# Kernel optimization log

Hardware: AMD Instinct MI355X
Metric: run time of the kernel (lower is better)

The kernel has to match this reference:

```python
import jax, jax.numpy as jnp
import numpy as np

B, T, D, H, E = 32, 512, 768, 12, 6  # batch, seq(=input_size), n_embd, num_heads, per-head dim
DFF = 4 * D
EPS = 1e-5


def setup_inputs() -> dict:
    key = jax.random.key(0)
    ks = jax.random.split(key, 10)
    s = 0.02
    return {
        "x": jax.random.normal(ks[0], (B, T, D), jnp.float32),
        "Wq": jax.random.normal(ks[1], (H, D, E), jnp.float32) * s,
        "Wk": jax.random.normal(ks[2], (H, D, E), jnp.float32) * s,
        "Wv": jax.random.normal(ks[3], (H, D, E), jnp.float32) * s,
        "Wo": jax.random.normal(ks[4], (H * E, D), jnp.float32) * s,
        "bo": jnp.zeros((D,), jnp.float32),
        "W1": jax.random.normal(ks[5], (D, DFF), jnp.float32) * s,
        "b1": jnp.zeros((DFF,), jnp.float32),
        "W2": jax.random.normal(ks[6], (DFF, D), jnp.float32) * s,
        "b2": jnp.zeros((D,), jnp.float32),
        "g1": jnp.ones((D,), jnp.float32),
        "beta1": jnp.zeros((D,), jnp.float32),
        "g2": jnp.ones((D,), jnp.float32),
        "beta2": jnp.zeros((D,), jnp.float32),
    }


def _layernorm(x, g, b):
    m = jnp.mean(x, axis=-1, keepdims=True)
    v = jnp.var(x, axis=-1, keepdims=True)  # biased, matches torch LayerNorm
    return (x - m) * jax.lax.rsqrt(v + EPS) * g + b


def reference(x, Wq, Wk, Wv, Wo, bo, W1, b1, W2, b2, g1, beta1, g2, beta2):
    # --- pre-LN multi-head causal attention (dropout = identity, eval mode) ---
    xn = _layernorm(x, g1, beta1)
    q = jnp.einsum("btd,hde->bhte", xn, Wq)
    k = jnp.einsum("btd,hde->bhte", xn, Wk)
    v = jnp.einsum("btd,hde->bhte", xn, Wv)
    scores = jnp.einsum("bhte,bhse->bhts", q, k) * (E ** -0.5)
    causal = jnp.tril(jnp.ones((T, T), dtype=bool))
    scores = jnp.where(causal, scores, -jnp.inf)
    w = jax.nn.softmax(scores, axis=-1)
    o = jnp.einsum("bhts,bhse->bhte", w, v)
    o = o.transpose(0, 2, 1, 3).reshape(B, T, H * E)  # concat heads -> [B,T,72]
    x = x + o @ Wo + bo
    # --- pre-LN feed-forward ---
    y = _layernorm(x, g2, beta2)
    ff = jax.nn.relu(y @ W1 + b1) @ W2 + b2
    return x + ff
```

## Files before the change

kernel.cpp:

```cpp
#include <hip/hip_runtime.h>
#include <hip/hip_bf16.h>

#define BT 16384
#define DIM 768
#define NH 12
#define DFF 3072

typedef __attribute__((ext_vector_type(8))) short short8;
typedef __attribute__((ext_vector_type(4))) float floatx4;
typedef __attribute__((ext_vector_type(4))) unsigned short ushort4b;

using bf16 = __hip_bfloat16;

static __device__ __forceinline__ float b2f(bf16 v) { return __bfloat162float(v); }
static __device__ __forceinline__ bf16 f2b(float v) { return __float2bfloat16(v); }
static __device__ __forceinline__ float blo(unsigned int u) { return __uint_as_float(u << 16); }
static __device__ __forceinline__ float bhi(unsigned int u) { return __uint_as_float(u & 0xffff0000u); }

static __device__ __forceinline__ void gload_lds16(const void* g, void* l) {
    __builtin_amdgcn_global_load_lds(
        (const __attribute__((address_space(1))) unsigned int*)g,
        (__attribute__((address_space(3))) unsigned int*)l, 16, 0, 0);
}

__global__ __launch_bounds__(256) void prep_kernel(
    const float* __restrict__ Wq, const float* __restrict__ Wk, const float* __restrict__ Wv,
    const float* __restrict__ Wo, const float* __restrict__ W1, const float* __restrict__ W2,
    bf16* __restrict__ wqkv, bf16* __restrict__ wo_t,
    bf16* __restrict__ w1t, bf16* __restrict__ w2t)
{
    const int z = blockIdx.z;
    if (z == 2) {
        int i = (blockIdx.y * 96 + blockIdx.x) * 256 + threadIdx.x;
        const int S0 = 256 * 768, S1 = 768 * 96;
        if (i < S0) {
            int c = i / 768, dd = i % 768;
            float v = 0.f;
            if (c < 216) {
                int sel = c / 72, cc = c % 72, h = cc / 6, e = cc % 6;
                const float* W = (sel == 0) ? Wq : (sel == 1) ? Wk : Wv;
                v = W[((size_t)h * 768 + dd) * 6 + e];
            }
            wqkv[i] = f2b(v);
        } else if ((i -= S0) < S1) {
            int n = i / 96, r = i % 96;
            wo_t[i] = f2b(r < 72 ? Wo[r * 768 + n] : 0.f);
        }
        return;
    }
    const float* in = z ? W2 : W1;
    bf16* out = z ? w2t : w1t;
    const int R = z ? 3072 : 768, C = z ? 768 : 3072;
    const int bx = z ? blockIdx.y : blockIdx.x;
    const int by = z ? blockIdx.x : blockIdx.y;
    __shared__ float t[32][33];
    int c0 = bx * 32, r0 = by * 32;
    int cx = threadIdx.x & 31, ry = threadIdx.x >> 5;
#pragma unroll
    for (int j = 0; j < 4; j++)
        t[ry + j * 8][cx] = in[(size_t)(r0 + ry + j * 8) * C + c0 + cx];
    __syncthreads();
    int rx = cx, cy = ry;
#pragma unroll
    for (int j = 0; j < 4; j++)
        out[(size_t)(c0 + cy + j * 8) * R + r0 + rx] = f2b(t[rx][cy + j * 8]);
}

__global__ __launch_bounds__(192) void ln_kernel(
    const float* __restrict__ x, const float* __restrict__ g, const float* __restrict__ be,
    bf16* __restrict__ out)
{
    int row = blockIdx.x;
    int tid = threadIdx.x;
    const float4* xr = (const float4*)(x + (size_t)row * DIM);
    float4 v = xr[tid];
    float s = v.x + v.y + v.z + v.w;
    float s2 = v.x * v.x + v.y * v.y + v.z * v.z + v.w * v.w;
#pragma unroll
    for (int off = 32; off; off >>= 1) {
        s += __shfl_down(s, off);
        s2 += __shfl_down(s2, off);
    }
    __shared__ float red[6];
    int wv = tid >> 6, ln = tid & 63;
    if (ln == 0) { red[wv] = s; red[3 + wv] = s2; }
    __syncthreads();
    float ts = red[0] + red[1] + red[2];
    float ts2 = red[3] + red[4] + red[5];
    float mean = ts * (1.f / 768.f);
    float var = ts2 * (1.f / 768.f) - mean * mean;
    float rstd = rsqrtf(var + 1e-5f);
    int c = tid * 4;
    float o0 = (v.x - mean) * rstd * g[c + 0] + be[c + 0];
    float o1 = (v.y - mean) * rstd * g[c + 1] + be[c + 1];
    float o2 = (v.z - mean) * rstd * g[c + 2] + be[c + 2];
    float o3 = (v.w - mean) * rstd * g[c + 3] + be[c + 3];
    bf16 h0 = f2b(o0), h1 = f2b(o1), h2 = f2b(o2), h3 = f2b(o3);
    ushort4b pk;
    pk[0] = *(unsigned short*)&h0; pk[1] = *(unsigned short*)&h1;
    pk[2] = *(unsigned short*)&h2; pk[3] = *(unsigned short*)&h3;
    *(ushort4b*)(out + (size_t)row * DIM + c) = pk;
}

template <int NSLAB, bool RELU, bool BIAS, bool RES, bool BF16OUT>
__global__ __launch_bounds__(256) void gemm_kernel(
    const bf16* __restrict__ A, const bf16* __restrict__ Bt,
    const float* __restrict__ bias, const float* __restrict__ res,
    void* __restrict__ Cv, int M, int N, int K)
{
    constexpr int SMEM_BYTES = BF16OUT ? (128 * 136 * 2) : (NSLAB * 2 * 128 * 32 * 2);
    __shared__ __align__(16) char smem[SMEM_BYTES];
    bf16* lA = (bf16*)smem;
    bf16* lB = lA + NSLAB * 128 * 32;

    const int tid = threadIdx.x;
    const int bm = blockIdx.x * 128;
    const int bn = blockIdx.y * 128;
    const int wave = tid >> 6, lane = tid & 63;
    const int wm = (wave >> 1) * 64, wn = (wave & 1) * 64;
    const int quad = lane >> 4, l16 = lane & 15;
    const int lrow = lane >> 2;
    const int lkc = (lane & 3) * 8;

    floatx4 acc[4][4] = {};

    for (int k0 = 0; k0 < K; k0 += NSLAB * 32) {
#pragma unroll
        for (int s = 0; s < NSLAB; s++) {
#pragma unroll
            for (int it = 0; it < 2; it++) {
                int r = wave * 32 + it * 16;
                gload_lds16(A + (size_t)(bm + r + lrow) * K + k0 + s * 32 + lkc,
                            lA + s * 4096 + r * 32);
                gload_lds16(Bt + (size_t)(bn + r + lrow) * K + k0 + s * 32 + lkc,
                            lB + s * 4096 + r * 32);
            }
        }
        __syncthreads();
#pragma unroll
        for (int s = 0; s < NSLAB; s++) {
            short8 af[4], bfr[4];
#pragma unroll
            for (int mt = 0; mt < 4; mt++)
                af[mt] = *(const short8*)(lA + s * 4096 + (wm + mt * 16 + l16) * 32 + quad * 8);
#pragma unroll
            for (int nt = 0; nt < 4; nt++)
                bfr[nt] = *(const short8*)(lB + s * 4096 + (wn + nt * 16 + l16) * 32 + quad * 8);
#pragma unroll
            for (int mt = 0; mt < 4; mt++)
#pragma unroll
                for (int nt = 0; nt < 4; nt++)
                    acc[mt][nt] = __builtin_amdgcn_mfma_f32_16x16x32_bf16(af[mt], bfr[nt], acc[mt][nt], 0, 0, 0);
        }
        __syncthreads();
    }

    if constexpr (BF16OUT) {
        bf16* ltile = (bf16*)smem;
#pragma unroll
        for (int mt = 0; mt < 4; mt++) {
#pragma unroll
            for (int nt = 0; nt < 4; nt++) {
                int tc = wn + nt * 16 + l16;
#pragma unroll
                for (int r = 0; r < 4; r++) {
                    int tr = wm + mt * 16 + quad * 4 + r;
                    float v0 = acc[mt][nt][r];
                    if constexpr (BIAS) v0 += bias[bn + tc];
                    if constexpr (RELU) v0 = fmaxf(v0, 0.f);
                    ltile[tr * 136 + tc] = f2b(v0);
                }
            }
        }
        __syncthreads();
        bf16* C = (bf16*)Cv;
        int rr0 = tid >> 4, col8 = (tid & 15) * 8;
        int gc = bn + col8;
#pragma unroll
        for (int p = 0; p < 8; p++) {
            int rr = p * 16 + rr0;
            if (gc < N)
                *(short8*)(C + (size_t)(bm + rr) * N + gc) =
                    *(const short8*)(ltile + rr * 136 + col8);
        }
    } else {
        float* C = (float*)Cv;
#pragma unroll
        for (int mt = 0; mt < 4; mt++) {
#pragma unroll
            for (int nt = 0; nt < 4; nt++) {
                int gc = bn + wn + nt * 16 + l16;
                if (gc < N) {
#pragma unroll
                    for (int r = 0; r < 4; r++) {
                        int gr = bm + wm + mt * 16 + quad * 4 + r;
                        float v0 = acc[mt][nt][r];
                        if constexpr (BIAS) v0 += bias[gc];
                        if constexpr (RES) v0 += res[(size_t)gr * N + gc];
                        if constexpr (RELU) v0 = fmaxf(v0, 0.f);
                        C[(size_t)gr * N + gc] = v0;
                    }
                }
            }
        }
    }
}

__global__ __launch_bounds__(512) void proj_ln_kernel(
    const bf16* __restrict__ o_pad, const bf16* __restrict__ wo_t,
    const float* __restrict__ bo, const float* __restrict__ x,
    const float* __restrict__ g, const float* __restrict__ be,
    float* __restrict__ x1, bf16* __restrict__ xn)
{
    extern __shared__ __align__(16) char smem[];
    bf16* pack = (bf16*)smem;
    float* rsum = (float*)(smem + 100352);
    float* rsq  = rsum + 256;
    float* mlds = rsq + 256;
    float* slds = mlds + 64;

    const int bm = blockIdx.x * 64;
    const int tid = threadIdx.x;
    const int w = tid >> 6, lane = tid & 63;
    const int wm = w >> 2, wn = w & 3;
    const int l16 = lane & 15, quad = lane >> 4;

    floatx4 acc[2][12] = {};
    short8 a[2][3];
#pragma unroll
    for (int mf = 0; mf < 2; mf++)
#pragma unroll
        for (int ks = 0; ks < 3; ks++)
            a[mf][ks] = *(const short8*)(o_pad +
                (size_t)(bm + wm * 32 + mf * 16 + l16) * 96 + ks * 32 + quad * 8);
#pragma unroll
    for (int nf = 0; nf < 12; nf++) {
        const int col = wn * 192 + nf * 16 + l16;
#pragma unroll
        for (int ks = 0; ks < 3; ks++) {
            short8 bfr = *(const short8*)(wo_t + (size_t)col * 96 + ks * 32 + quad * 8);
#pragma unroll
            for (int mf = 0; mf < 2; mf++)
                acc[mf][nf] = __builtin_amdgcn_mfma_f32_16x16x32_bf16(
                    a[mf][ks], bfr, acc[mf][nf], 0, 0, 0);
        }
    }
    float bov[12], gv[12], bev[12];
#pragma unroll
    for (int nf = 0; nf < 12; nf++) {
        const int gc = wn * 192 + nf * 16 + l16;
        bov[nf] = bo[gc]; gv[nf] = g[gc]; bev[nf] = be[gc];
    }
    float psum[2][4] = {}, psq[2][4] = {};
#pragma unroll
    for (int nf = 0; nf < 12; nf++) {
        const int gc = wn * 192 + nf * 16 + l16;
#pragma unroll
        for (int mf = 0; mf < 2; mf++) {
            const int gr = bm + wm * 32 + mf * 16 + quad * 4;
#pragma unroll
            for (int rr = 0; rr < 4; rr++) {
                float v = acc[mf][nf][rr] + bov[nf] + x[(size_t)(gr + rr) * 768 + gc];
                acc[mf][nf][rr] = v;
                x1[(size_t)(gr + rr) * 768 + gc] = v;
                psum[mf][rr] += v;
                psq[mf][rr] = fmaf(v, v, psq[mf][rr]);
            }
        }
    }
#pragma unroll
    for (int mf = 0; mf < 2; mf++)
#pragma unroll
        for (int rr = 0; rr < 4; rr++)
#pragma unroll
            for (int m = 1; m < 16; m <<= 1) {
                psum[mf][rr] += __shfl_xor(psum[mf][rr], m);
                psq[mf][rr]  += __shfl_xor(psq[mf][rr], m);
            }
    if (l16 == 0) {
#pragma unroll
        for (int mf = 0; mf < 2; mf++)
#pragma unroll
            for (int rr = 0; rr < 4; rr++) {
                int row = wm * 32 + mf * 16 + quad * 4 + rr;
                rsum[wn * 64 + row] = psum[mf][rr];
                rsq [wn * 64 + row] = psq[mf][rr];
            }
    }
    __syncthreads();
    if (tid < 64) {
        float s  = rsum[tid] + rsum[64 + tid] + rsum[128 + tid] + rsum[192 + tid];
        float s2 = rsq [tid] + rsq [64 + tid] + rsq [128 + tid] + rsq [192 + tid];
        float mean = s * (1.f / 768.f);
        float var = s2 * (1.f / 768.f) - mean * mean;
        mlds[tid] = mean;
        slds[tid] = rsqrtf(var + 1e-5f);
    }
    __syncthreads();
#pragma unroll
    for (int mf = 0; mf < 2; mf++)
#pragma unroll
        for (int rr = 0; rr < 4; rr++) {
            const int row = wm * 32 + mf * 16 + quad * 4 + rr;
            const float mean = mlds[row], rstd = slds[row];
#pragma unroll
            for (int nf = 0; nf < 12; nf++) {
                const int gc = wn * 192 + nf * 16 + l16;
                float v = (acc[mf][nf][rr] - mean) * rstd * gv[nf] + bev[nf];
                pack[row * 784 + gc] = f2b(v);
            }
        }
    __syncthreads();
#pragma unroll
    for (int it = 0; it < 12; it++) {
        int c = it * 512 + tid;
        int rr = c / 96, cc = (c - rr * 96) * 8;
        *(short8*)(xn + (size_t)(bm + rr) * 768 + cc) = *(const short8*)(pack + rr * 784 + cc);
    }
}

template <bool RELU, bool BIAS, bool RES, bool BF16OUT>
__global__ __launch_bounds__(512, 2) void gemm256_kernel(
    const bf16* __restrict__ A, const bf16* __restrict__ Bt,
    const float* __restrict__ bias, const float* __restrict__ res,
    void* __restrict__ Cv, int M, int N, int K)
{
    extern __shared__ __align__(16) char smem[];
    const int NT = K >> 6;
    const int k8 = blockIdx.x & 7, q = blockIdx.x >> 3;
    const int bm = (k8 * 8 + (q & 7)) << 8;
    const int bn = (q >> 3) << 8;

    const int tid = threadIdx.x;
    const int w = tid >> 6, lane = tid & 63;
    const int wm = w >> 2, wn = w & 3;
    const int l16 = lane & 15, quad = lane >> 4;

    const int rstg = (w >> 1) * 16 + (lane >> 2);
    const int cstg = (w & 1) * 32 + ((((lane & 3) * 8)) ^ ((lane & 32) ? 16 : 0));
    const bf16* aSrc = A + (size_t)(bm + rstg) * K + cstg;
    const bf16* bSrc = Bt + (size_t)(bn + rstg) * K + cstg;
    char* dstBase = smem + w * 1024;

    const int xr = (quad * 16) ^ ((l16 & 8) ? 32 : 0);
    const int aOff = wm * 16384 + l16 * 64 + xr;
    const int bOff = 32768 + wn * 8192 + l16 * 64 + xr;

#define STAGE(P, ISB, H, T) { \
    const bf16* _s = ((ISB) ? bSrc : aSrc) + ((size_t)((H) * 128) * K + (size_t)(T) * 64); \
    char* _d = dstBase + (P) * 65536 + (ISB) * 32768 + (H) * 16384; \
    gload_lds16(_s, _d); \
    gload_lds16(_s + (size_t)64 * K, _d + 8192); }

#define BARX() asm volatile("s_barrier" ::: "memory")
#define VMW(N_) asm volatile("s_waitcnt vmcnt(" #N_ ")" ::: "memory")

    floatx4 acc[8][4] = {};
    short8 a[4][2], b[2][2][2];

#define LDA_FM(QM, FM, CB) { _Pragma("unroll") for (int s = 0; s < 2; s++) \
        a[FM][s] = *(const short8*)((CB) + aOff + (QM) * 8192 + (FM) * 2048 + s * 1024); }
#define LDA(QM, CB) { LDA_FM(QM, 0, CB); LDA_FM(QM, 1, CB); LDA_FM(QM, 2, CB); LDA_FM(QM, 3, CB); }
#define LDB(QN, CB) { _Pragma("unroll") for (int fn = 0; fn < 2; fn++) { \
    _Pragma("unroll") for (int s = 0; s < 2; s++) \
        b[QN][fn][s] = *(const short8*)((CB) + bOff + (QN) * 4096 + fn * 2048 + s * 1024); } }
#define MMQ(QM, QN, FM) { __builtin_amdgcn_s_setprio(1); \
    _Pragma("unroll") for (int fn = 0; fn < 2; fn++) { \
    _Pragma("unroll") for (int s = 0; s < 2; s++) \
        acc[(QM)*4+(FM)][(QN)*2+fn] = __builtin_amdgcn_mfma_f32_16x16x32_bf16( \
            a[FM][s], b[QN][fn][s], acc[(QM)*4+(FM)][(QN)*2+fn], 0, 0, 0); } \
    __builtin_amdgcn_s_setprio(0); }
#define MM(QM, QN) { MMQ(QM, QN, 0); MMQ(QM, QN, 1); MMQ(QM, QN, 2); MMQ(QM, QN, 3); }

    STAGE(0, 0, 0, 0); STAGE(0, 0, 1, 0); STAGE(0, 1, 0, 0); STAGE(0, 1, 1, 0);
    STAGE(1, 0, 0, 1); STAGE(1, 0, 1, 1); STAGE(1, 1, 0, 1); STAGE(1, 1, 1, 1);
    VMW(8);
    BARX();
    LDB(0, smem); LDA(0, smem);

    for (int g = 0; g < NT; ++g) {
        const int p = g & 1;
        const char* cb = smem + p * 65536;
        const char* nb = smem + ((p ^ 1) * 65536);
        LDB(1, cb);
        MM(0, 0);
        BARX();
        MMQ(0, 1, 0); LDA_FM(1, 0, cb);
        MMQ(0, 1, 1); LDA_FM(1, 1, cb);
        MMQ(0, 1, 2); LDA_FM(1, 2, cb);
        MMQ(0, 1, 3); LDA_FM(1, 3, cb);
        VMW(0);
        BARX();
        if (g + 2 < NT) { STAGE(p, 1, 0, g + 2); STAGE(p, 1, 1, g + 2); }
        MM(1, 1);
        BARX();
        if (g + 2 < NT) { STAGE(p, 0, 0, g + 2); STAGE(p, 0, 1, g + 2); }
        if (g + 1 < NT) {
            MMQ(1, 0, 0); LDA_FM(0, 0, nb);
            MMQ(1, 0, 1); LDA_FM(0, 1, nb);
            MMQ(1, 0, 2); LDA_FM(0, 2, nb);
            MMQ(1, 0, 3); LDA_FM(0, 3, nb);
            LDB(0, nb);
        } else {
            MM(1, 0);
        }
        BARX();
    }

    if constexpr (BF16OUT) {
        bf16* lt = (bf16*)smem;
#pragma unroll
        for (int RF = 0; RF < 8; RF++) {
            const int row = wm * 128 + (RF >> 2) * 64 + (RF & 3) * 16 + quad * 4;
#pragma unroll
            for (int CF = 0; CF < 4; CF++) {
                const int col = wn * 64 + (CF >> 1) * 32 + (CF & 1) * 16 + l16;
                float bv = BIAS ? bias[bn + col] : 0.f;
#pragma unroll
                for (int rr = 0; rr < 4; rr++) {
                    float v = acc[RF][CF][rr] + bv;
                    if constexpr (RELU) v = fmaxf(v, 0.f);
                    lt[(row + rr) * 280 + col] = f2b(v);
                }
            }
        }
        asm volatile("s_waitcnt lgkmcnt(0)" ::: "memory");
        BARX();
        bf16* C = (bf16*)Cv;
#pragma unroll
        for (int it = 0; it < 16; it++) {
            int c = it * 512 + tid;
            int rr = c >> 5, c8 = (c & 31) * 8;
            *(short8*)(C + (size_t)(bm + rr) * N + bn + c8) =
                *(const short8*)(lt + rr * 280 + c8);
        }
    } else {
        float* C = (float*)Cv;
#pragma unroll
        for (int RF = 0; RF < 8; RF++) {
            const int gr = bm + wm * 128 + (RF >> 2) * 64 + (RF & 3) * 16 + quad * 4;
#pragma unroll
            for (int CF = 0; CF < 4; CF++) {
                const int gc = bn + wn * 64 + (CF >> 1) * 32 + (CF & 1) * 16 + l16;
                float bv = BIAS ? bias[gc] : 0.f;
#pragma unroll
                for (int rr = 0; rr < 4; rr++) {
                    float v = acc[RF][CF][rr] + bv;
                    if constexpr (RES) v += res[(size_t)(gr + rr) * N + gc];
                    if constexpr (RELU) v = fmaxf(v, 0.f);
                    C[(size_t)(gr + rr) * N + gc] = v;
                }
            }
        }
    }
#undef STAGE
#undef BARX
#undef VMW
#undef LDA_FM
#undef LDA
#undef LDB
#undef MMQ
#undef MM
}

template <int NTC, int TPB, bool RELU, bool BIAS, bool RES, bool BF16OUT>
__global__ __launch_bounds__(512, 2) void gemm192_kernel(
    const bf16* __restrict__ A, const bf16* __restrict__ Bt,
    const float* __restrict__ bias, const float* __restrict__ res,
    void* __restrict__ Cv, int N)
{
    constexpr int KC = NTC * 64;
    constexpr int NG = NTC * TPB;
    extern __shared__ __align__(16) char smem[];

    const int k8 = blockIdx.x & 7, q = blockIdx.x >> 3;
    const int sid = (q >> 3) * 64 + k8 * 8 + (q & 7);
    const int bm = (sid & 63) << 8;
    const int bnBase = (sid >> 6) * (TPB * 192);

    const int tid = threadIdx.x;
    const int w = tid >> 6, lane = tid & 63;
    const int wm = w >> 1, wn = w & 1;
    const int l16 = lane & 15, quad = lane >> 4;

    const int rstg = (w >> 1) * 16 + (lane >> 2);
    const int cstg = (w & 1) * 32 + (((lane & 3) * 8) ^ ((lane & 32) ? 16 : 0));
    const bf16* aSrc = A + (size_t)(bm + rstg) * KC + cstg;
    const bf16* bSrc = Bt + (size_t)(bnBase + rstg) * KC + cstg;
    const int stgoff = w * 1024;

    const int xr = (quad * 16) ^ ((l16 & 8) ? 32 : 0);
    const int aoff = wm * 8192 + l16 * 64 + xr;
    const int boff = 32768 + wn * 12288 + l16 * 64 + xr;

#define STG2(BO, ISB, CH) gload_lds16( \
        ((ISB) ? bS2 : aS2) + (size_t)(CH) * 64 * KC, \
        smem + (BO) + (ISB) * 32768 + (CH) * 8192 + stgoff)

#define BARX() asm volatile("s_barrier" ::: "memory")
#define VMW(N_) asm volatile("s_waitcnt vmcnt(" #N_ ")" ::: "memory")

    floatx4 acc[4][6] = {};
    short8 a[2][2][2], b[2][3][2];

#define LDA(QM, CB) { _Pragma("unroll") for (int fm = 0; fm < 2; fm++) { \
    _Pragma("unroll") for (int s = 0; s < 2; s++) \
        a[QM][fm][s] = *(const short8*)((CB) + aoff + (QM) * 4096 + fm * 2048 + s * 1024); } }
#define LDB(QN, CB) { _Pragma("unroll") for (int fn = 0; fn < 3; fn++) { \
    _Pragma("unroll") for (int s = 0; s < 2; s++) \
        b[QN][fn][s] = *(const short8*)((CB) + boff + (QN) * 6144 + fn * 2048 + s * 1024); } }
#define MM(QM, QN) { __builtin_amdgcn_s_setprio(1); \
    _Pragma("unroll") for (int fm = 0; fm < 2; fm++) { \
    _Pragma("unroll") for (int fn = 0; fn < 3; fn++) { \
    _Pragma("unroll") for (int s = 0; s < 2; s++) \
        acc[(QM)*2+fm][(QN)*3+fn] = __builtin_amdgcn_mfma_f32_16x16x32_bf16( \
            a[QM][fm][s], b[(QN)][fn][s], acc[(QM)*2+fm][(QN)*3+fn], 0, 0, 0); } } \
    __builtin_amdgcn_s_setprio(0); }

    {
        const bf16* aS2 = aSrc;           const bf16* bS2 = bSrc;
#pragma unroll
        for (int c = 0; c < 4; c++) STG2(0, 0, c);
#pragma unroll
        for (int c = 0; c < 3; c++) STG2(0, 1, c);
        aS2 = aSrc + 64; bS2 = bSrc + 64;
#pragma unroll
        for (int c = 0; c < 4; c++) STG2(57344, 0, c);
#pragma unroll
        for (int c = 0; c < 3; c++) STG2(57344, 1, c);
    }
    VMW(7);
    BARX();
    LDA(0, smem); LDB(0, smem);

    for (int G = 0; G < NG; ++G) {
        const int bo = (G & 1) * 57344;
        const char* cb = smem + bo;
        const char* nb = smem + (bo ^ 57344);
        const int v = G + 2;
        const bf16* aS2 = aSrc;
        const bf16* bS2 = bSrc;
        if (v < NG) {
            const int t2 = v / NTC, g2 = v - t2 * NTC;
            aS2 = aSrc + (size_t)g2 * 64;
            bS2 = bSrc + (size_t)t2 * (192 * (size_t)KC) + (size_t)g2 * 64;
        }
        LDA(1, cb);
        MM(0, 0);
        BARX();
        LDB(1, cb);
        MM(1, 0);
        VMW(0);
        BARX();
        if (v < NG) { STG2(bo, 0, 0); STG2(bo, 0, 1); STG2(bo, 0, 2); STG2(bo, 0, 3); }
        if (G + 1 < NG) LDB(0, nb);
        MM(1, 1);
        BARX();
        if (v < NG) { STG2(bo, 1, 0); STG2(bo, 1, 1); STG2(bo, 1, 2); }
        MM(0, 1);
        if (G + 1 < NG) LDA(0, nb);
        BARX();
    }

    if constexpr (!BF16OUT) {
        float* C = (float*)Cv;
        const int bn = bnBase;
#pragma unroll
        for (int mf = 0; mf < 4; mf++) {
            const int gr = bm + wm * 64 + mf * 16 + quad * 4;
#pragma unroll
            for (int nf = 0; nf < 6; nf++) {
                const int gc = bn + wn * 96 + nf * 16 + l16;
                float bv = BIAS ? bias[gc] : 0.f;
#pragma unroll
                for (int r = 0; r < 4; r++) {
                    float v = acc[mf][nf][r] + bv;
                    if constexpr (RES) v += res[(size_t)(gr + r) * N + gc];
                    if constexpr (RELU) v = fmaxf(v, 0.f);
                    C[(size_t)(gr + r) * N + gc] = v;
                }
            }
        }
    }
#undef STG2
#undef BARX
#undef VMW
#undef LDA
#undef LDB
#undef MM
}

__global__ __launch_bounds__(256) void attn_kernel(const bf16* __restrict__ qkv, bf16* __restrict__ o_pad)
{
    int blk = blockIdx.x;
    int half = blk & 1;
    int bh = blk >> 1;
    int b = bh / NH, h = bh % NH;
    int wave = threadIdx.x >> 6, lane = threadIdx.x & 63;
    const int jmap0[4] = {0, 2, 5, 7}, jmap1[4] = {1, 3, 4, 6};
    int j = half ? jmap1[wave] : jmap0[wave];
    int t = j * 64 + lane;
    int smax = half ? 448 : 512;

    __shared__ uint4 ks8[512];
    __shared__ uint4 vs8[512];
    const bf16* base = qkv + (size_t)b * 512 * 216;
    for (int s = threadIdx.x; s < smax; s += 256) {
        const unsigned int* kp = (const unsigned int*)(base + s * 216 + 72 + h * 6);
        const unsigned int* vp = (const unsigned int*)(base + s * 216 + 144 + h * 6);
        ks8[s] = make_uint4(kp[0], kp[1], kp[2], 0u);
        vs8[s] = make_uint4(vp[0], vp[1], vp[2], 0u);
    }
    __syncthreads();

    const float kSc = 0.4082482904638630f * 1.4426950408889634f;
    const unsigned int* qp = (const unsigned int*)(base + t * 216 + h * 6);
    unsigned int q01 = qp[0], q23 = qp[1], q45 = qp[2];
    float q0 = blo(q01) * kSc, q1 = bhi(q01) * kSc;
    float q2 = blo(q23) * kSc, q3 = bhi(q23) * kSc;
    float q4 = blo(q45) * kSc, q5 = bhi(q45) * kSc;

    float l = 0.f;
    float o0 = 0, o1 = 0, o2 = 0, o3 = 0, o4 = 0, o5 = 0;
    for (int s = 0; s <= t; s++) {
        uint4 kk = ks8[s];
        float sc = q0 * blo(kk.x);
        sc = fmaf(q1, bhi(kk.x), sc);
        sc = fmaf(q2, blo(kk.y), sc);
        sc = fmaf(q3, bhi(kk.y), sc);
        sc = fmaf(q4, blo(kk.z), sc);
        sc = fmaf(q5, bhi(kk.z), sc);
        float p = exp2f(sc);
        l += p;
        uint4 vv = vs8[s];
        o0 = fmaf(p, blo(vv.x), o0);
        o1 = fmaf(p, bhi(vv.x), o1);
        o2 = fmaf(p, blo(vv.y), o2);
        o3 = fmaf(p, bhi(vv.y), o3);
        o4 = fmaf(p, blo(vv.z), o4);
        o5 = fmaf(p, bhi(vv.z), o5);
    }
    float inv = 1.f / l;
    bf16* orow = o_pad + (size_t)(b * 512 + t) * 96 + h * 6;
    orow[0] = f2b(o0 * inv);
    orow[1] = f2b(o1 * inv);
    orow[2] = f2b(o2 * inv);
    orow[3] = f2b(o3 * inv);
    orow[4] = f2b(o4 * inv);
    orow[5] = f2b(o5 * inv);
}

extern "C" void kernel_launch(void* const* d_in, const int* in_sizes, int n_in,
                              void* d_out, int out_size, void* d_ws, size_t ws_size,
                              hipStream_t stream)
{
    const float* x   = (const float*)d_in[0];
    const float* Wq  = (const float*)d_in[1];
    const float* Wk  = (const float*)d_in[2];
    const float* Wv  = (const float*)d_in[3];
    const float* Wo  = (const float*)d_in[4];
    const float* bo  = (const float*)d_in[5];
    const float* W1  = (const float*)d_in[6];
    const float* b1  = (const float*)d_in[7];
    const float* W2  = (const float*)d_in[8];
    const float* b2  = (const float*)d_in[9];
    const float* g1  = (const float*)d_in[10];
    const float* be1 = (const float*)d_in[11];
    const float* g2  = (const float*)d_in[12];
    const float* be2 = (const float*)d_in[13];

    char* ws = (char*)d_ws;
    size_t off = 0;
    auto alloc = [&](size_t bytes) {
        void* p = ws + off;
        off = (off + bytes + 255) & ~(size_t)255;
        return p;
    };
    bf16*  xn    = (bf16*)alloc((size_t)BT * DIM * 2);
    bf16*  qkvb  = (bf16*)alloc((size_t)BT * 216 * 2);
    bf16*  o_pad = (bf16*)alloc((size_t)BT * 96 * 2);
    float* x1    = (float*)alloc((size_t)BT * DIM * 4);
    bf16*  ffb   = (bf16*)alloc((size_t)BT * DFF * 2);
    bf16*  wqkv  = (bf16*)alloc((size_t)256 * 768 * 2);
    bf16*  wo_t  = (bf16*)alloc((size_t)768 * 96 * 2);
    bf16*  w1t   = (bf16*)alloc((size_t)3072 * 768 * 2);
    bf16*  w2t   = (bf16*)alloc((size_t)768 * 3072 * 2);

    hipFuncSetAttribute(reinterpret_cast<const void*>(&gemm256_kernel<true, true, false, true>),
                        hipFuncAttributeMaxDynamicSharedMemorySize, 256 * 280 * 2);
    hipFuncSetAttribute(reinterpret_cast<const void*>(&gemm192_kernel<48, 1, false, true, true, false>),
                        hipFuncAttributeMaxDynamicSharedMemorySize, 114688);
    hipFuncSetAttribute(reinterpret_cast<const void*>(&proj_ln_kernel),
                        hipFuncAttributeMaxDynamicSharedMemorySize, 103488);

    prep_kernel<<<dim3(96, 24, 3), 256, 0, stream>>>(Wq, Wk, Wv, Wo, W1, W2,
                                                     wqkv, wo_t, w1t, w2t);

    ln_kernel<<<BT, 192, 0, stream>>>(x, g1, be1, xn);
    gemm_kernel<2, false, false, false, true><<<dim3(128, 2), 256, 0, stream>>>(
        xn, wqkv, nullptr, nullptr, qkvb, BT, 216, 768);
    attn_kernel<<<32 * NH * 2, 256, 0, stream>>>(qkvb, o_pad);
    proj_ln_kernel<<<256, 512, 103488, stream>>>(o_pad, wo_t, bo, x, g2, be2, x1, xn);
    gemm256_kernel<true, true, false, true><<<768, 512, 256 * 280 * 2, stream>>>(
        xn, w1t, b1, nullptr, ffb, BT, 3072, 768);
    gemm192_kernel<48, 1, false, true, true, false><<<256, 512, 114688, stream>>>(
        ffb, w2t, b2, x1, (float*)d_out, 768);
}
```

Before: 408.9 us.

## Restructure GEMM main loop to two barriers per step with reordered stage prefetch

```diff
diff --git a/kernel.cpp b/kernel.cpp
--- a/kernel.cpp
+++ b/kernel.cpp
@@ -372,37 +372,33 @@
     __builtin_amdgcn_s_setprio(0); }
 #define MM(QM, QN) { MMQ(QM, QN, 0); MMQ(QM, QN, 1); MMQ(QM, QN, 2); MMQ(QM, QN, 3); }
 
-    STAGE(0, 0, 0, 0); STAGE(0, 0, 1, 0); STAGE(0, 1, 0, 0); STAGE(0, 1, 1, 0);
-    STAGE(1, 0, 0, 1); STAGE(1, 0, 1, 1); STAGE(1, 1, 0, 1); STAGE(1, 1, 1, 1);
-    VMW(8);
+    STAGE(0, 1, 0, 0); STAGE(0, 1, 1, 0);
+    STAGE(0, 0, 0, 0); STAGE(0, 0, 1, 0);
+    STAGE(1, 1, 0, 1); STAGE(1, 1, 1, 1);
+    VMW(4);
     BARX();
-    LDB(0, smem); LDA(0, smem);
+    LDB(0, smem); LDB(1, smem); LDA(0, smem);
 
     for (int g = 0; g < NT; ++g) {
         const int p = g & 1;
         const char* cb = smem + p * 65536;
         const char* nb = smem + ((p ^ 1) * 65536);
-        LDB(1, cb);
-        MM(0, 0);
-        BARX();
-        MMQ(0, 1, 0); LDA_FM(1, 0, cb);
-        MMQ(0, 1, 1); LDA_FM(1, 1, cb);
-        MMQ(0, 1, 2); LDA_FM(1, 2, cb);
-        MMQ(0, 1, 3); LDA_FM(1, 3, cb);
+        if (g + 1 < NT) { STAGE(p ^ 1, 0, 0, g + 1); STAGE(p ^ 1, 0, 1, g + 1); }
+        MMQ(0, 0, 0); MMQ(0, 1, 0); LDA_FM(1, 0, cb);
+        MMQ(0, 0, 1); MMQ(0, 1, 1); LDA_FM(1, 1, cb);
+        MMQ(0, 0, 2); MMQ(0, 1, 2); LDA_FM(1, 2, cb);
+        MMQ(0, 0, 3); MMQ(0, 1, 3); LDA_FM(1, 3, cb);
         VMW(0);
         BARX();
         if (g + 2 < NT) { STAGE(p, 1, 0, g + 2); STAGE(p, 1, 1, g + 2); }
-        MM(1, 1);
-        BARX();
-        if (g + 2 < NT) { STAGE(p, 0, 0, g + 2); STAGE(p, 0, 1, g + 2); }
         if (g + 1 < NT) {
-            MMQ(1, 0, 0); LDA_FM(0, 0, nb);
-            MMQ(1, 0, 1); LDA_FM(0, 1, nb);
-            MMQ(1, 0, 2); LDA_FM(0, 2, nb);
-            MMQ(1, 0, 3); LDA_FM(0, 3, nb);
-            LDB(0, nb);
+            MMQ(1, 1, 0); MMQ(1, 0, 0); LDA_FM(0, 0, nb);
+            MMQ(1, 1, 1); MMQ(1, 0, 1); LDA_FM(0, 1, nb);
+            MMQ(1, 1, 2); MMQ(1, 0, 2); LDA_FM(0, 2, nb);
+            MMQ(1, 1, 3); MMQ(1, 0, 3); LDA_FM(0, 3, nb);
+            LDB(0, nb); LDB(1, nb);
         } else {
-            MM(1, 0);
+            MM(1, 1); MM(1, 0);
         }
         BARX();
     }
```

New measurement: 490.0 us. 19.8% more time.
